# Optimization experiments

Measured on AMD Instinct MI355X. Metric: run time of the kernel, lower is better.

The kernel has to match this reference:

```python
import jax, jax.numpy as jnp
import numpy as np
import math

B, C, L_SEQ, PRED = 32, 21, 512, 96
D, H, DFF, NLAYERS = 512, 8, 2048, 3
E = D // H
PATCH_LEN, STRIDE, PAD = 16, 8, 8
PATCH_NUM = (L_SEQ - PATCH_LEN) // STRIDE + 2  # 64
MA = 25          # moving-average kernel of series_decomp
FACTOR = 1
TOP_K = int(FACTOR * math.log(PATCH_NUM))  # top-k delays in AutoCorrelation


def _pos_embedding(max_len, d_model):
    pos = np.arange(max_len, dtype=np.float32)[:, None]
    div = np.exp(np.arange(0, d_model, 2, dtype=np.float32) * -(math.log(10000.0) / d_model))
    pe = np.zeros((max_len, d_model), np.float32)
    pe[:, 0::2] = np.sin(pos * div)
    pe[:, 1::2] = np.cos(pos * div)
    return jnp.asarray(pe)

POS_EMB = _pos_embedding(PATCH_NUM, D)


def setup_inputs():
    key = jax.random.key(0)
    ks = iter(jax.random.split(key, 48))
    g = lambda shape, s=0.02: jax.random.normal(next(ks), shape, jnp.float32) * s
    inp = {"x_enc": jax.random.normal(next(ks), (B, L_SEQ, C), jnp.float32)}
    inp["w_val"] = g((PATCH_LEN, D))  # PatchEmbedding value_embedding (no bias)
    for tag in ("ac", "sa"):
        for nm in ("Wq", "Wk", "Wv", "Wo"):
            inp[nm + "_" + tag] = g((NLAYERS, D, D))
        for nm in ("bq", "bk", "bv", "bo"):
            inp[nm + "_" + tag] = g((NLAYERS, D))
    inp["Wf"] = g((NLAYERS, 2 * D, D))
    inp["bf"] = g((NLAYERS, D))
    inp["W1"] = g((NLAYERS, D, DFF))   # conv1 (1x1, no bias)
    inp["W2"] = g((NLAYERS, DFF, D))   # conv2 (1x1, no bias)
    inp["bn_g"] = jnp.ones((D,), jnp.float32)
    inp["bn_b"] = jnp.zeros((D,), jnp.float32)
    inp["W_head"] = g((D * PATCH_NUM, PRED))
    inp["b_head"] = g((PRED,))
    return inp


def _proj_heads(x, W, b):
    N, L, _ = x.shape
    return (x @ W + b).reshape(N, L, H, E)


def _auto_corr(x, Wq, bq, Wk, bk, Wv, bv, Wo, bo):
    # AutoCorrelation (training-mode time_delay_agg): FFT correlation + top-k roll aggregation
    N, L, _ = x.shape
    q = _proj_heads(x, Wq, bq)
    k = _proj_heads(x, Wk, bk)
    v = _proj_heads(x, Wv, bv)
    qf = jnp.fft.rfft(q.transpose(0, 2, 3, 1), axis=-1)   # [N,H,E,Lf]
    kf = jnp.fft.rfft(k.transpose(0, 2, 3, 1), axis=-1)
    corr = jnp.fft.irfft(qf * jnp.conj(kf), n=L, axis=-1)  # [N,H,E,L]
    vals = v.transpose(0, 2, 3, 1)                          # [N,H,E,L]
    mean_corr = corr.mean(axis=(1, 2))                      # [N,L]
    _, top_idx = jax.lax.top_k(mean_corr.mean(axis=0), TOP_K)  # delays shared across batch
    w = jax.nn.softmax(mean_corr[:, top_idx], axis=-1)      # [N,TOP_K]
    rolled = jax.vmap(lambda s: jnp.roll(vals, -s, axis=-1))(top_idx)  # [K,N,H,E,L]
    agg = jnp.einsum('knhel,nk->nhel', rolled, w)
    return agg.transpose(0, 3, 1, 2).reshape(N, L, D) @ Wo + bo


def _full_attn(x, Wq, bq, Wk, bk, Wv, bv, Wo, bo):
    N, L, _ = x.shape
    q = _proj_heads(x, Wq, bq)
    k = _proj_heads(x, Wk, bk)
    v = _proj_heads(x, Wv, bv)
    scores = jnp.einsum('blhe,bshe->bhls', q, k) / math.sqrt(E)
    out = jnp.einsum('bhls,bshe->blhe', jax.nn.softmax(scores, axis=-1), v)
    return out.reshape(N, L, D) @ Wo + bo


def _decomp(x):
    # series_decomp: residual after edge-replicated moving average (returns seasonal part)
    half = (MA - 1) // 2
    xp = jnp.concatenate([jnp.repeat(x[:, :1], half, axis=1), x,
                          jnp.repeat(x[:, -1:], half, axis=1)], axis=1)
    cs = jnp.cumsum(xp, axis=1)
    cs = jnp.concatenate([jnp.zeros_like(cs[:, :1]), cs], axis=1)
    mean = (cs[:, MA:] - cs[:, :-MA]) / MA
    return x - mean


def _forward(x_enc, w_val, Wq_ac, bq_ac, Wk_ac, bk_ac, Wv_ac, bv_ac, Wo_ac, bo_ac,
             Wq_sa, bq_sa, Wk_sa, bk_sa, Wv_sa, bv_sa, Wo_sa, bo_sa,
             Wf, bf, W1, W2, bn_g, bn_b, W_head, b_head):
    # instance normalization over time
    means = x_enc.mean(axis=1, keepdims=True)                 # [B,1,C]
    xc = x_enc - means
    stdev = jnp.sqrt(xc.var(axis=1, keepdims=True) + 1e-5)    # [B,1,C]
    xn = xc / stdev
    # patch embedding (channel independent): replication-pad end, unfold, linear + pos emb
    xp = xn.transpose(0, 2, 1)                                # [B,C,L]
    xp = jnp.concatenate([xp, jnp.repeat(xp[..., -1:], PAD, axis=-1)], axis=-1)
    idx = jnp.arange(PATCH_NUM)[:, None] * STRIDE + jnp.arange(PATCH_LEN)[None, :]
    patches = xp[..., idx]                                    # [B,C,P,patch_len]
    x = patches.reshape(B * C, PATCH_NUM, PATCH_LEN) @ w_val + POS_EMB  # [B*C,P,D]
    # hybrid encoder layers
    for l in range(NLAYERS):
        a = _auto_corr(x, Wq_ac[l], bq_ac[l], Wk_ac[l], bk_ac[l], Wv_ac[l], bv_ac[l], Wo_ac[l], bo_ac[l])
        s = _full_attn(x, Wq_sa[l], bq_sa[l], Wk_sa[l], bk_sa[l], Wv_sa[l], bv_sa[l], Wo_sa[l], bo_sa[l])
        fused = jnp.concatenate([a, s], axis=-1) @ Wf[l] + bf[l]
        x = _decomp(x + fused)
        y = jax.nn.relu(x @ W1[l]) @ W2[l]                    # 1x1 convs == pointwise linears
        x = _decomp(x + y)
    # final BatchNorm1d over d_model channels (batch statistics, affine)
    mu = x.mean(axis=(0, 1))
    var = x.var(axis=(0, 1))
    x = (x - mu) / jnp.sqrt(var + 1e-5) * bn_g + bn_b
    # head: [B*C,P,D] -> [B,C,D,P] -> flat (d-major) -> pred_len
    enc = x.reshape(B, C, PATCH_NUM, D).transpose(0, 1, 3, 2).reshape(B, C, D * PATCH_NUM)
    dec = (enc @ W_head + b_head).transpose(0, 2, 1)          # [B,PRED,C]
    return dec * stdev[:, 0][:, None, :] + means[:, 0][:, None, :]


def reference(x_enc, w_val, Wq_ac, bq_ac, Wk_ac, bk_ac, Wv_ac, bv_ac, Wo_ac, bo_ac,
              Wq_sa, bq_sa, Wk_sa, bk_sa, Wv_sa, bv_sa, Wo_sa, bo_sa,
              Wf, bf, W1, W2, bn_g, bn_b, W_head, b_head):
    return _forward(x_enc, w_val, Wq_ac, bq_ac, Wk_ac, bk_ac, Wv_ac, bv_ac, Wo_ac, bo_ac,
                    Wq_sa, bq_sa, Wk_sa, bk_sa, Wv_sa, bv_sa, Wo_sa, bo_sa,
                    Wf, bf, W1, W2, bn_g, bn_b, W_head, b_head)
```

## Files before the change

kernel.cpp:

```cpp
#include <hip/hip_runtime.h>
#include <math.h>


typedef unsigned short u16;
typedef short s16x8 __attribute__((ext_vector_type(8)));
typedef u16 u16x8 __attribute__((ext_vector_type(8)));
typedef float f32x4 __attribute__((ext_vector_type(4)));

#define MROWS 43008
#define NSEQ  672

__device__ __forceinline__ float bf2f(u16 b) {
  union { unsigned u; float f; } v; v.u = ((unsigned)b) << 16; return v.f;
}
__device__ __forceinline__ u16 f2bf(float f) {
  union { float f; unsigned u; } v; v.f = f;
  unsigned r = v.u + 0x7FFFu + ((v.u >> 16) & 1u);
  return (u16)(r >> 16);
}

__device__ __forceinline__ void gload16(const u16* g, u16* l) {
  __builtin_amdgcn_global_load_lds(
      (const __attribute__((address_space(1))) unsigned int*)g,
      (__attribute__((address_space(3))) unsigned int*)l, 16, 0, 0);
}

__global__ __launch_bounds__(256) void zero_out_kernel(float* __restrict__ o, int n) {
  int i = blockIdx.x * 256 + threadIdx.x;
  if (i < n) o[i] = 0.f;
}

__global__ __launch_bounds__(256) void transpose_cvt_b(
    const float* __restrict__ W, u16* __restrict__ Wt, int K, int N,
    long long sW, long long sT) {
  __shared__ float t[32][33];
  int z = blockIdx.z;
  W += (size_t)z * sW;
  Wt += (size_t)z * sT;
  int k0 = blockIdx.x * 32, n0 = blockIdx.y * 32;
  int tx = threadIdx.x, ty = threadIdx.y;
#pragma unroll
  for (int i = 0; i < 32; i += 8)
    t[ty + i][tx] = W[(size_t)(k0 + ty + i) * N + n0 + tx];
  __syncthreads();
#pragma unroll
  for (int i = 0; i < 32; i += 8)
    Wt[(size_t)(n0 + ty + i) * K + k0 + tx] = f2bf(t[tx][ty + i]);
}

__global__ __launch_bounds__(256) void transpose_cvt_six(
    const float* __restrict__ Wq_sa, const float* __restrict__ Wk_sa,
    const float* __restrict__ Wv_sa, const float* __restrict__ Wq_ac,
    const float* __restrict__ Wk_ac, const float* __restrict__ Wv_ac,
    u16* __restrict__ dst) {
  __shared__ float t[32][33];
  int z = blockIdx.z;
  int l = z / 6, wi = z % 6;
  const float* srcs[6] = {Wq_sa, Wk_sa, Wv_sa, Wq_ac, Wk_ac, Wv_ac};
  const float* W = srcs[wi] + (size_t)l * 262144;
  u16* out = dst + ((size_t)l * 6 + wi) * 262144;
  int k0 = blockIdx.x * 32, n0 = blockIdx.y * 32;
  int tx = threadIdx.x, ty = threadIdx.y;
#pragma unroll
  for (int i = 0; i < 32; i += 8)
    t[ty + i][tx] = W[(size_t)(k0 + ty + i) * 512 + n0 + tx];
  __syncthreads();
#pragma unroll
  for (int i = 0; i < 32; i += 8)
    out[(size_t)(n0 + ty + i) * 512 + k0 + tx] = f2bf(t[tx][ty + i]);
}

__global__ __launch_bounds__(256) void cvt_bf16_nine(
    const float* __restrict__ Wo_ac, const float* __restrict__ Wo_sa,
    const float* __restrict__ Wv_ac, u16* __restrict__ dst) {
  int z = blockIdx.z;
  int l = z / 3, s = z % 3;
  const float* base = (s == 0) ? Wo_ac : (s == 1 ? Wo_sa : Wv_ac);
  const float* src = base + (size_t)l * 262144;
  u16* out = dst + ((size_t)l * 3 + s) * 262144;
  int i = blockIdx.x * 256 + threadIdx.x;
  if (i < 262144) out[i] = f2bf(src[i]);
}

__global__ __launch_bounds__(512) void boa_eff_kernel(
    const float* __restrict__ Wo_ac, const float* __restrict__ bo_ac,
    const float* __restrict__ bv_ac, float* __restrict__ out) {
  int l = blockIdx.x;
  int i = threadIdx.x;
  const float* Wo = Wo_ac + (size_t)l * 262144;
  float s = bo_ac[l * 512 + i];
  for (int k = 0; k < 512; k++) s += bv_ac[l * 512 + k] * Wo[(size_t)k * 512 + i];
  out[l * 512 + i] = s;
}

__global__ __launch_bounds__(512) void bias_combine(
    const float* __restrict__ WfW, const float* __restrict__ bfW,
    const float* __restrict__ boa_eff, const float* __restrict__ bo_sa,
    float* __restrict__ out) {
  int l = blockIdx.x;
  const float* Wf = WfW + (size_t)l * 524288;
  int n = threadIdx.x;
  float s = bfW[l * 512 + n];
  for (int i = 0; i < 512; i++) s += boa_eff[l * 512 + i] * Wf[(size_t)i * 512 + n];
  for (int i = 0; i < 512; i++) s += bo_sa[l * 512 + i] * Wf[(size_t)(512 + i) * 512 + n];
  out[l * 512 + n] = s;
}

__global__ __launch_bounds__(512) void gemm256p(
    const u16* __restrict__ A1, const u16* __restrict__ A2, int lda, int ksplit,
    const u16* __restrict__ Bt, int ldb,
    const float* __restrict__ b0, const float* __restrict__ b1,
    const float* __restrict__ b2,
    u16* __restrict__ C, int ldc, int K, int relu, int nb) {
  __shared__ u16 smA[2][2][256 * 32];
  __shared__ u16 smB[2][2][256 * 32];
  int g = blockIdx.x;
  if ((gridDim.x & 7) == 0) g = (g & 7) * (gridDim.x >> 3) + (g >> 3);
  int m0 = (g / nb) * 256, n0 = (g % nb) * 256;
  int tid = threadIdx.x, lane = tid & 63, wid = tid >> 6;
  int wr = wid >> 2, wc = wid & 3;
  int m_in = lane & 15, kq = lane >> 4;
  int srow0 = lane >> 2, sslot = lane & 3;

  f32x4 acc[8][4];
#pragma unroll
  for (int i = 0; i < 8; i++)
#pragma unroll
    for (int j = 0; j < 4; j++) acc[i][j] = (f32x4){0.f, 0.f, 0.f, 0.f};

  int nt = K >> 6;

  auto STAGE = [&](int tp, int t, int kh) {
    int k0 = t * 64 + kh * 32;
    const u16* Ap; int kk;
    if (t * 64 < ksplit) { Ap = A1; kk = k0; } else { Ap = A2; kk = k0 - ksplit; }
#pragma unroll
    for (int i = 0; i < 2; i++) {
      int r = i * 128 + wid * 16 + srow0;
      int gs = (sslot ^ ((r >> 1) & 3)) * 8;
      gload16(&Ap[(size_t)(m0 + r) * lda + kk + gs],
              &smA[tp][kh][(i * 128 + wid * 16) * 32]);
      gload16(&Bt[(size_t)(n0 + r) * ldb + k0 + gs],
              &smB[tp][kh][(i * 128 + wid * 16) * 32]);
    }
  };

  STAGE(0, 0, 0);
  STAGE(0, 0, 1);
  asm volatile("s_waitcnt vmcnt(4)" ::: "memory");
  asm volatile("s_barrier" ::: "memory");

  int tp = 0;
  for (int t = 0; t < nt; ++t) {
    int tn = t + 1 < nt ? t + 1 : t;
#pragma unroll
    for (int kh = 0; kh < 2; kh++) {
      const u16* As = &smA[tp][kh][0];
      const u16* Bs = &smB[tp][kh][0];
      s16x8 a_[8], b_[4];
#pragma unroll
      for (int mf = 0; mf < 8; mf++) {
        int row = wr * 128 + mf * 16 + m_in;
        a_[mf] = *(const s16x8*)&As[row * 32 + ((kq ^ ((row >> 1) & 3)) * 8)];
      }
#pragma unroll
      for (int nf = 0; nf < 4; nf++) {
        int row = wc * 64 + nf * 16 + m_in;
        b_[nf] = *(const s16x8*)&Bs[row * 32 + ((kq ^ ((row >> 1) & 3)) * 8)];
      }
      STAGE(tp ^ 1, tn, kh);
      asm volatile("s_waitcnt vmcnt(4)" ::: "memory");
      asm volatile("s_barrier" ::: "memory");
      __builtin_amdgcn_s_setprio(1);
#pragma unroll
      for (int mf = 0; mf < 8; mf++)
#pragma unroll
        for (int nf = 0; nf < 4; nf++)
          acc[mf][nf] = __builtin_amdgcn_mfma_f32_16x16x32_bf16(
              a_[mf], b_[nf], acc[mf][nf], 0, 0, 0);
      __builtin_amdgcn_s_setprio(0);
    }
    tp ^= 1;
  }
  int r0 = m0 + wr * 128 + (kq << 2);
#pragma unroll
  for (int mf = 0; mf < 8; mf++) {
#pragma unroll
    for (int nf = 0; nf < 4; nf++) {
      int col = n0 + wc * 64 + nf * 16 + m_in;
      const float* bp = (col < 512) ? b0 : (col < 1024 ? b1 : b2);
      float bv = bp ? bp[col & 511] : 0.f;
#pragma unroll
      for (int r = 0; r < 4; r++) {
        float v = acc[mf][nf][r] + bv;
        if (relu) v = fmaxf(v, 0.f);
        C[(size_t)(r0 + mf * 16 + r) * ldc + col] = f2bf(v);
      }
    }
  }
}

__global__ __launch_bounds__(256) void gemm128p(
    const u16* __restrict__ A1, const u16* __restrict__ A2, int lda, int ksplit,
    const u16* __restrict__ Bt, int ldb,
    const float* __restrict__ b0, const float* __restrict__ b1,
    const float* __restrict__ b2,
    u16* __restrict__ C, int ldc, int K, int relu, int nb) {
  __shared__ u16 sm[3][8192];
  int g = blockIdx.x;
  if ((gridDim.x & 7) == 0) g = (g & 7) * (gridDim.x >> 3) + (g >> 3);
  int m0 = (g / nb) * 128, n0 = (g % nb) * 128;
  int tid = threadIdx.x, lane = tid & 63, w = tid >> 6;
  int wr = w >> 1, wc = w & 1;
  int srow = w * 16 + (lane >> 2);
  int scol = (((lane & 3) ^ ((lane >> 3) & 3)) * 8);
  int m_in = lane & 15;
  int sgrp = lane >> 4;
  int offA[4], offB[4];
#pragma unroll
  for (int mf = 0; mf < 4; mf++) {
    int row = wr * 64 + mf * 16 + m_in;
    offA[mf] = row * 32 + ((sgrp ^ ((row >> 1) & 3)) * 8);
  }
#pragma unroll
  for (int nf = 0; nf < 4; nf++) {
    int row = wc * 64 + nf * 16 + m_in;
    offB[nf] = 4096 + row * 32 + ((sgrp ^ ((row >> 1) & 3)) * 8);
  }
  f32x4 acc[4][4];
#pragma unroll
  for (int i = 0; i < 4; i++)
#pragma unroll
    for (int j = 0; j < 4; j++) acc[i][j] = (f32x4){0.f, 0.f, 0.f, 0.f};

  int nt = K >> 5;
  auto STAGE = [&](int b, int t) {
    int k0 = t * 32;
    const u16* Ab; int kk;
    if (k0 < ksplit) { Ab = A1; kk = k0; } else { Ab = A2; kk = k0 - ksplit; }
    u16* base = &sm[b][0];
    gload16(&Ab[(size_t)(m0 + srow) * lda + kk + scol],      base + w * 512);
    gload16(&Ab[(size_t)(m0 + 64 + srow) * lda + kk + scol], base + 2048 + w * 512);
    gload16(&Bt[(size_t)(n0 + srow) * ldb + k0 + scol],      base + 4096 + w * 512);
    gload16(&Bt[(size_t)(n0 + 64 + srow) * ldb + k0 + scol], base + 6144 + w * 512);
  };

  STAGE(0, 0);
  STAGE(1, 1 < nt ? 1 : nt - 1);
  int cb = 0;
  for (int t = 0; t < nt; ++t) {
    int pf = t + 2 < nt ? t + 2 : nt - 1;
    int pb = cb + 2 >= 3 ? cb - 1 : cb + 2;
    STAGE(pb, pf);
    asm volatile("s_waitcnt vmcnt(8)" ::: "memory");
    asm volatile("s_barrier" ::: "memory");
    const u16* lb = &sm[cb][0];
    s16x8 a_[4], b_[4];
#pragma unroll
    for (int mf = 0; mf < 4; mf++) a_[mf] = *(const s16x8*)&lb[offA[mf]];
#pragma unroll
    for (int nf = 0; nf < 4; nf++) b_[nf] = *(const s16x8*)&lb[offB[nf]];
    __builtin_amdgcn_s_setprio(1);
#pragma unroll
    for (int mf = 0; mf < 4; mf++)
#pragma unroll
      for (int nf = 0; nf < 4; nf++)
        acc[mf][nf] = __builtin_amdgcn_mfma_f32_16x16x32_bf16(
            a_[mf], b_[nf], acc[mf][nf], 0, 0, 0);
    __builtin_amdgcn_s_setprio(0);
    asm volatile("s_barrier" ::: "memory");
    cb = cb + 1 >= 3 ? 0 : cb + 1;
  }
  int r0 = m0 + wr * 64 + (sgrp << 2);
  int cl = lane & 15;
#pragma unroll
  for (int mf = 0; mf < 4; mf++) {
#pragma unroll
    for (int nf = 0; nf < 4; nf++) {
      int col = n0 + wc * 64 + nf * 16 + cl;
      const float* bp = (col < 512) ? b0 : (col < 1024 ? b1 : b2);
      float bv = bp ? bp[col & 511] : 0.f;
#pragma unroll
      for (int r = 0; r < 4; r++) {
        float v = acc[mf][nf][r] + bv;
        if (relu) v = fmaxf(v, 0.f);
        C[(size_t)(r0 + mf * 16 + r) * ldc + col] = f2bf(v);
      }
    }
  }
}

__global__ __launch_bounds__(256) void gram_mc_kernel(
    const u16* __restrict__ Q, const u16* __restrict__ K, int ld,
    float* __restrict__ MC) {
  __shared__ u16 lA[64][40];
  __shared__ u16 lB[64][40];
  __shared__ float red[64];
  int n = blockIdx.x;
  int tid = threadIdx.x, lane = tid & 63, w = tid >> 6;
  int sr = tid >> 2, scol = (tid & 3) * 8;
  if (tid < 64) red[tid] = 0.f;
  f32x4 acc[4];
#pragma unroll
  for (int i = 0; i < 4; i++) acc[i] = (f32x4){0.f, 0.f, 0.f, 0.f};
  size_t base = (size_t)n * 64 * ld;
  for (int k0 = 0; k0 < 512; k0 += 32) {
    *(u16x8*)&lA[sr][scol] = *(const u16x8*)&Q[base + (size_t)sr * ld + k0 + scol];
    *(u16x8*)&lB[sr][scol] = *(const u16x8*)&K[base + (size_t)sr * ld + k0 + scol];
    __syncthreads();
    int ar = w * 16 + (lane & 15);
    int kk = (lane >> 4) * 8;
    s16x8 af = *(const s16x8*)&lA[ar][kk];
#pragma unroll
    for (int nb = 0; nb < 4; nb++) {
      s16x8 bfr = *(const s16x8*)&lB[nb * 16 + (lane & 15)][kk];
      acc[nb] = __builtin_amdgcn_mfma_f32_16x16x32_bf16(af, bfr, acc[nb], 0, 0, 0);
    }
    __syncthreads();
  }
  int row0 = w * 16 + ((lane >> 4) << 2);
  int cl = lane & 15;
#pragma unroll
  for (int nb = 0; nb < 4; nb++) {
    int col = nb * 16 + cl;
#pragma unroll
    for (int r = 0; r < 4; r++)
      atomicAdd(&red[(row0 + r - col) & 63], acc[nb][r]);
  }
  __syncthreads();
  if (tid < 64) MC[n * 64 + tid] = red[tid] * (1.f / 512.f);
}

__global__ __launch_bounds__(256) void instnorm_kernel(
    const float* __restrict__ xe, float* __restrict__ MEANS, float* __restrict__ STDEV) {
  int n = blockIdx.x;
  int b = n / 21, c = n % 21;
  int tid = threadIdx.x;
  float v0 = xe[((size_t)b * 512 + tid) * 21 + c];
  float v1 = xe[((size_t)b * 512 + tid + 256) * 21 + c];
  float s = v0 + v1, ss = v0 * v0 + v1 * v1;
  for (int o = 32; o; o >>= 1) { s += __shfl_down(s, o); ss += __shfl_down(ss, o); }
  __shared__ float rs[4], rss[4];
  if ((tid & 63) == 0) { rs[tid >> 6] = s; rss[tid >> 6] = ss; }
  __syncthreads();
  if (tid == 0) {
    s = rs[0] + rs[1] + rs[2] + rs[3];
    ss = rss[0] + rss[1] + rss[2] + rss[3];
    float mean = s * (1.f / 512.f);
    float var = ss * (1.f / 512.f) - mean * mean;
    MEANS[n] = mean;
    STDEV[n] = sqrtf(var + 1e-5f);
  }
}

__global__ __launch_bounds__(256) void pe_kernel(float* __restrict__ PE) {
  int i = blockIdx.x * 256 + threadIdx.x;
  int p = i >> 9, d = i & 511;
  int k = d >> 1;
  float freq = expf(-(float)(2 * k) * (9.210340371976184f / 512.f));
  float ang = (float)p * freq;
  PE[i] = (d & 1) ? cosf(ang) : sinf(ang);
}

__global__ __launch_bounds__(256) void patch_kernel(
    const float* __restrict__ xe, const float* __restrict__ wv,
    const float* __restrict__ PE, const float* __restrict__ MEANS,
    const float* __restrict__ STDEV, u16* __restrict__ X) {
  __shared__ float pw[16][512];
  __shared__ float pat[8][16];
  int bx = blockIdx.x;
  int n = bx >> 3, pb = bx & 7;
  int b = n / 21, c = n % 21;
  int tid = threadIdx.x;
  float mean = MEANS[n], inv = 1.f / STDEV[n];
  for (int i = tid; i < 8192; i += 256) pw[i >> 9][i & 511] = wv[i];
  if (tid < 128) {
    int pp = tid >> 4, j = tid & 15;
    int l = (pb * 8 + pp) * 8 + j;
    if (l > 511) l = 511;
    pat[pp][j] = (xe[((size_t)b * 512 + l) * 21 + c] - mean) * inv;
  }
  __syncthreads();
  for (int i = tid; i < 4096; i += 256) {
    int pp = i >> 9, d = i & 511;
    int p = pb * 8 + pp;
    float s = PE[p * 512 + d];
#pragma unroll
    for (int j = 0; j < 16; j++) s += pat[pp][j] * pw[j][d];
    X[((size_t)n * 64 + p) * 512 + d] = f2bf(s);
  }
}

__global__ __launch_bounds__(256) void topk_softw_kernel(
    const float* __restrict__ MC, int* __restrict__ TIDX, float* __restrict__ WSM) {
  __shared__ float g[256];
  __shared__ float gt[64];
  __shared__ int dly[4];
  int tid = threadIdx.x;
  int tau = tid & 63, part = tid >> 6;
  float s = 0.f;
  for (int n = part * 168; n < (part + 1) * 168; n++) s += MC[n * 64 + tau];
  g[tid] = s;
  __syncthreads();
  if (tid < 64) gt[tid] = g[tid] + g[64 + tid] + g[128 + tid] + g[192 + tid];
  __syncthreads();
  if (tid == 0) {
    for (int j = 0; j < 4; j++) {
      int best = 0; float bv = -1e30f;
      for (int t = 0; t < 64; t++) if (gt[t] > bv) { bv = gt[t]; best = t; }
      dly[j] = best;
      TIDX[j] = best;
      gt[best] = -1e30f;
    }
  }
  __syncthreads();
  for (int n = tid; n < 672; n += 256) {
    float v[4], mx = -1e30f;
#pragma unroll
    for (int j = 0; j < 4; j++) { v[j] = MC[n * 64 + dly[j]]; mx = fmaxf(mx, v[j]); }
    float ssum = 0.f;
#pragma unroll
    for (int j = 0; j < 4; j++) { v[j] = __expf(v[j] - mx); ssum += v[j]; }
    float inv = 1.f / ssum;
#pragma unroll
    for (int j = 0; j < 4; j++) WSM[n * 4 + j] = v[j] * inv;
  }
}

__global__ __launch_bounds__(256) void agg_kernel(
    const u16* __restrict__ V, int ldv, const float* __restrict__ WSM,
    const int* __restrict__ TIDX, u16* __restrict__ OUT, int ldo) {
  int n = blockIdx.x;
  __shared__ float w[4];
  __shared__ int dly[4];
  int tid = threadIdx.x;
  if (tid < 4) { w[tid] = WSM[n * 4 + tid]; dly[tid] = TIDX[tid]; }
  __syncthreads();
  for (int i = tid; i < 64 * 512; i += 256) {
    int l = i >> 9, d = i & 511;
    float s = 0.f;
#pragma unroll
    for (int j = 0; j < 4; j++)
      s += w[j] * bf2f(V[((size_t)n * 64 + ((l + dly[j]) & 63)) * ldv + d]);
    OUT[((size_t)n * 64 + l) * ldo + d] = f2bf(s);
  }
}

__global__ __launch_bounds__(256) void attn_mfma(u16* __restrict__ QKV) {
  __shared__ u16 lq[64][72], lk[64][72], lvt[64][72], lp[64][72];
  int n = blockIdx.x >> 3, h = blockIdx.x & 7;
  size_t base = (size_t)n * 64 * 1536;
  int qo = h * 64, ko = 512 + h * 64, vo = 1024 + h * 64;
  int tid = threadIdx.x, lane = tid & 63, w = tid >> 6;
  int r = tid >> 2, c0 = (tid & 3) * 16;
  *(u16x8*)&lq[r][c0]     = *(const u16x8*)&QKV[base + (size_t)r * 1536 + qo + c0];
  *(u16x8*)&lq[r][c0 + 8] = *(const u16x8*)&QKV[base + (size_t)r * 1536 + qo + c0 + 8];
  *(u16x8*)&lk[r][c0]     = *(const u16x8*)&QKV[base + (size_t)r * 1536 + ko + c0];
  *(u16x8*)&lk[r][c0 + 8] = *(const u16x8*)&QKV[base + (size_t)r * 1536 + ko + c0 + 8];
  u16x8 v0 = *(const u16x8*)&QKV[base + (size_t)r * 1536 + vo + c0];
  u16x8 v1 = *(const u16x8*)&QKV[base + (size_t)r * 1536 + vo + c0 + 8];
#pragma unroll
  for (int j = 0; j < 8; j++) { lvt[c0 + j][r] = v0[j]; lvt[c0 + 8 + j][r] = v1[j]; }
  __syncthreads();
  int m_in = lane & 15, ks = (lane >> 4) * 8;
  int rq = lane >> 4;
  s16x8 aq0 = *(const s16x8*)&lq[w * 16 + m_in][ks];
  s16x8 aq1 = *(const s16x8*)&lq[w * 16 + m_in][32 + ks];
  f32x4 s4[4];
#pragma unroll
  for (int nf = 0; nf < 4; nf++) {
    s4[nf] = (f32x4){0.f, 0.f, 0.f, 0.f};
    s16x8 b0 = *(const s16x8*)&lk[nf * 16 + m_in][ks];
    s16x8 b1 = *(const s16x8*)&lk[nf * 16 + m_in][32 + ks];
    s4[nf] = __builtin_amdgcn_mfma_f32_16x16x32_bf16(aq0, b0, s4[nf], 0, 0, 0);
    s4[nf] = __builtin_amdgcn_mfma_f32_16x16x32_bf16(aq1, b1, s4[nf], 0, 0, 0);
  }
  float mx[4] = {-1e30f, -1e30f, -1e30f, -1e30f};
#pragma unroll
  for (int nf = 0; nf < 4; nf++)
#pragma unroll
    for (int r4 = 0; r4 < 4; r4++) {
      s4[nf][r4] *= 0.125f;
      mx[r4] = fmaxf(mx[r4], s4[nf][r4]);
    }
#pragma unroll
  for (int o = 1; o < 16; o <<= 1)
#pragma unroll
    for (int r4 = 0; r4 < 4; r4++) mx[r4] = fmaxf(mx[r4], __shfl_xor(mx[r4], o));
  float sum[4] = {0.f, 0.f, 0.f, 0.f};
#pragma unroll
  for (int nf = 0; nf < 4; nf++)
#pragma unroll
    for (int r4 = 0; r4 < 4; r4++) {
      float e = __expf(s4[nf][r4] - mx[r4]);
      s4[nf][r4] = e;
      sum[r4] += e;
    }
#pragma unroll
  for (int o = 1; o < 16; o <<= 1)
#pragma unroll
    for (int r4 = 0; r4 < 4; r4++) sum[r4] += __shfl_xor(sum[r4], o);
#pragma unroll
  for (int nf = 0; nf < 4; nf++)
#pragma unroll
    for (int r4 = 0; r4 < 4; r4++)
      lp[w * 16 + rq * 4 + r4][nf * 16 + m_in] = f2bf(s4[nf][r4] / sum[r4]);
  __syncthreads();
  s16x8 ap0 = *(const s16x8*)&lp[w * 16 + m_in][ks];
  s16x8 ap1 = *(const s16x8*)&lp[w * 16 + m_in][32 + ks];
#pragma unroll
  for (int nf = 0; nf < 4; nf++) {
    f32x4 o4 = (f32x4){0.f, 0.f, 0.f, 0.f};
    s16x8 b0 = *(const s16x8*)&lvt[nf * 16 + m_in][ks];
    s16x8 b1 = *(const s16x8*)&lvt[nf * 16 + m_in][32 + ks];
    o4 = __builtin_amdgcn_mfma_f32_16x16x32_bf16(ap0, b0, o4, 0, 0, 0);
    o4 = __builtin_amdgcn_mfma_f32_16x16x32_bf16(ap1, b1, o4, 0, 0, 0);
#pragma unroll
    for (int r4 = 0; r4 < 4; r4++)
      QKV[base + (size_t)(w * 16 + rq * 4 + r4) * 1536 + qo + nf * 16 + m_in] =
          f2bf(o4[r4]);
  }
}

__global__ __launch_bounds__(256) void decomp_kernel(
    u16* __restrict__ X, const u16* __restrict__ DELTA, int ds) {
  int n = blockIdx.x >> 1;
  int d = ((blockIdx.x & 1) << 8) + threadIdx.x;
  size_t xb = ((size_t)n * 64) * 512 + d;
  size_t db = ((size_t)n * 64) * ds + d;
  float v[64];
#pragma unroll
  for (int l = 0; l < 64; l++)
    v[l] = bf2f(X[xb + (size_t)l * 512]) + bf2f(DELTA[db + (size_t)l * ds]);
  float s = 12.f * v[0];
#pragma unroll
  for (int t = 0; t <= 12; t++) s += v[t];
#pragma unroll
  for (int l = 0; l < 64; l++) {
    float out = v[l] - s * (1.f / 25.f);
    X[xb + (size_t)l * 512] = f2bf(out);
    if (l < 63) {
      int add = l + 13; if (add > 63) add = 63;
      int sub = l - 12; if (sub < 0) sub = 0;
      s += v[add] - v[sub];
    }
  }
}

__global__ __launch_bounds__(256) void bn_part(
    const u16* __restrict__ X, float* __restrict__ PS) {
  int ch = blockIdx.x, tid = threadIdx.x;
  float s1a = 0, s2a = 0, s1b = 0, s2b = 0;
  size_t base = (size_t)ch * 128 * 512;
  for (int r = 0; r < 128; r++) {
    float a = bf2f(X[base + (size_t)r * 512 + tid]);
    float b = bf2f(X[base + (size_t)r * 512 + tid + 256]);
    s1a += a; s2a += a * a; s1b += b; s2b += b * b;
  }
  PS[(size_t)(ch * 2 + 0) * 512 + tid] = s1a;
  PS[(size_t)(ch * 2 + 0) * 512 + tid + 256] = s1b;
  PS[(size_t)(ch * 2 + 1) * 512 + tid] = s2a;
  PS[(size_t)(ch * 2 + 1) * 512 + tid + 256] = s2b;
}

__global__ __launch_bounds__(256) void bn_final(
    const float* __restrict__ PS, const float* __restrict__ g,
    const float* __restrict__ b, float* __restrict__ SCALE, float* __restrict__ SHIFT) {
  int d = blockIdx.x * 256 + threadIdx.x;
  float s = 0, ss = 0;
  for (int c = 0; c < 336; c++) {
    s += PS[(size_t)(c * 2) * 512 + d];
    ss += PS[(size_t)(c * 2 + 1) * 512 + d];
  }
  float mu = s * (1.f / 43008.f);
  float var = ss * (1.f / 43008.f) - mu * mu;
  float inv = 1.f / sqrtf(var + 1e-5f);
  float sc = g[d] * inv;
  SCALE[d] = sc;
  SHIFT[d] = b[d] - mu * sc;
}

__global__ __launch_bounds__(256) void bn_transpose_kernel(
    const u16* __restrict__ X, const float* __restrict__ SCALE,
    const float* __restrict__ SHIFT, u16* __restrict__ ENC) {
  __shared__ u16 t[64][72];
  int n = blockIdx.x >> 3, dc = (blockIdx.x & 7) * 64;
  int tid = threadIdx.x;
  for (int i = tid; i < 4096; i += 256) {
    int p = i >> 6, d = i & 63;
    float v = bf2f(X[((size_t)n * 64 + p) * 512 + dc + d]) * SCALE[dc + d] + SHIFT[dc + d];
    t[p][d] = f2bf(v);
  }
  __syncthreads();
  for (int i = tid; i < 4096; i += 256) {
    int d = i >> 6, p = i & 63;
    ENC[(size_t)n * 32768 + (size_t)(dc + d) * 64 + p] = t[p][d];
  }
}

__global__ __launch_bounds__(256) void head_gemm(
    const u16* __restrict__ ENC, const u16* __restrict__ Wht,
    float* __restrict__ PART) {
  __shared__ u16 lA[64][40];
  __shared__ u16 lB[96][40];
  int bm = blockIdx.x;
  int kc = blockIdx.y;
  int tid = threadIdx.x, lane = tid & 63, w = tid >> 6;
  int sr = tid >> 2, sc0 = (tid & 3) * 8;
  f32x4 acc[6];
#pragma unroll
  for (int i = 0; i < 6; i++) acc[i] = (f32x4){0.f, 0.f, 0.f, 0.f};
  for (int kk0 = 0; kk0 < 2048; kk0 += 32) {
    int k0 = kc * 2048 + kk0;
    *(u16x8*)&lA[sr][sc0] =
        *(const u16x8*)&ENC[(size_t)(bm * 64 + sr) * 32768 + k0 + sc0];
    for (int i = tid; i < 96 * 4; i += 256) {
      int rB = i >> 2, seg = (i & 3) * 8;
      *(u16x8*)&lB[rB][seg] = *(const u16x8*)&Wht[(size_t)rB * 32768 + k0 + seg];
    }
    __syncthreads();
    int ar = w * 16 + (lane & 15);
    int kk = (lane >> 4) * 8;
    s16x8 af = *(const s16x8*)&lA[ar][kk];
#pragma unroll
    for (int nb = 0; nb < 6; nb++) {
      s16x8 bfr = *(const s16x8*)&lB[nb * 16 + (lane & 15)][kk];
      acc[nb] = __builtin_amdgcn_mfma_f32_16x16x32_bf16(af, bfr, acc[nb], 0, 0, 0);
    }
    __syncthreads();
  }
  int rb = bm * 64 + w * 16 + ((lane >> 4) << 2);
  int cl = lane & 15;
#pragma unroll
  for (int nb = 0; nb < 6; nb++) {
    int col = nb * 16 + cl;
#pragma unroll
    for (int r = 0; r < 4; r++) {
      int row = rb + r;
      if (row < 672) PART[((size_t)kc * 672 + row) * 96 + col] = acc[nb][r];
    }
  }
}

__global__ __launch_bounds__(256) void head_reduce(
    const float* __restrict__ PART, const float* __restrict__ bh,
    const float* __restrict__ STDEV, const float* __restrict__ MEANS,
    float* __restrict__ OUT) {
  int i = blockIdx.x * 256 + threadIdx.x;
  if (i >= 672 * 96) return;
  int n = i / 96, r = i % 96;
  float s = bh[r];
  for (int kc = 0; kc < 16; kc++) s += PART[((size_t)kc * 672 + n) * 96 + r];
  int b = n / 21, c = n % 21;
  OUT[((size_t)b * 96 + r) * 21 + c] = s * STDEV[n] + MEANS[n];
}

extern "C" void kernel_launch(void* const* d_in, const int* in_sizes, int n_in,
                              void* d_out, int out_size, void* d_ws, size_t ws_size,
                              hipStream_t stream) {
  const float* x_enc = (const float*)d_in[0];
  const float* w_val = (const float*)d_in[1];
  const float* Wq_ac = (const float*)d_in[2];
  const float* Wk_ac = (const float*)d_in[3];
  const float* Wv_ac = (const float*)d_in[4];
  const float* Wo_ac = (const float*)d_in[5];
  const float* bq_ac = (const float*)d_in[6];
  const float* bk_ac = (const float*)d_in[7];
  const float* bv_ac = (const float*)d_in[8];
  const float* bo_ac = (const float*)d_in[9];
  const float* Wq_sa = (const float*)d_in[10];
  const float* Wk_sa = (const float*)d_in[11];
  const float* Wv_sa = (const float*)d_in[12];
  const float* Wo_sa = (const float*)d_in[13];
  const float* bq_sa = (const float*)d_in[14];
  const float* bk_sa = (const float*)d_in[15];
  const float* bv_sa = (const float*)d_in[16];
  const float* bo_sa = (const float*)d_in[17];
  const float* WfW   = (const float*)d_in[18];
  const float* bfW   = (const float*)d_in[19];
  const float* W1    = (const float*)d_in[20];
  const float* W2    = (const float*)d_in[21];
  const float* bn_g  = (const float*)d_in[22];
  const float* bn_b  = (const float*)d_in[23];
  const float* W_head = (const float*)d_in[24];
  const float* b_head = (const float*)d_in[25];
  (void)in_sizes; (void)n_in; (void)out_size;

  char* wsp = (char*)d_ws;
  size_t off = 0;
  auto alloc = [&](size_t bytes) -> void* {
    void* p = wsp + off;
    off += (bytes + 255) & ~(size_t)255;
    return p;
  };
  u16* X    = (u16*)alloc((size_t)MROWS * 512 * 2);
  u16* Q3   = (u16*)alloc((size_t)MROWS * 1536 * 2);
  u16* SIX   = (u16*)alloc((size_t)3 * 6 * 262144 * 2);
  u16* W1T   = (u16*)alloc((size_t)3 * 1048576 * 2);
  u16* W2T   = (u16*)alloc((size_t)3 * 1048576 * 2);
  u16* WFT   = (u16*)alloc((size_t)3 * 524288 * 2);
  u16* WORIG = (u16*)alloc((size_t)3 * 3 * 262144 * 2);
  u16* WCOMB = (u16*)alloc((size_t)3 * 524288 * 2);
  u16* WHT   = (u16*)alloc((size_t)3145728 * 2);
  u16* TMP   = (u16*)alloc((size_t)262144 * 2);
  float* PE = (float*)alloc((size_t)32768 * 4);
  float* MEANS = (float*)alloc(672 * 4);
  float* STDEV = (float*)alloc(672 * 4);
  float* MC = (float*)alloc(672 * 64 * 4);
  int* TIDX = (int*)alloc(4 * 4);
  float* WSM = (float*)alloc(672 * 4 * 4);
  float* BNP = (float*)alloc((size_t)336 * 1024 * 4);
  float* SCALE = (float*)alloc(512 * 4);
  float* SHIFT = (float*)alloc(512 * 4);
  float* BOAE = (float*)alloc(3 * 512 * 4);
  float* BCOMB = (float*)alloc(3 * 512 * 4);
  u16* C0 = Q3;
  u16* C1 = Q3 + 512;
  u16* C2 = Q3 + 1024;
  u16* HBUF = Q3;
  u16* YBUF = Q3 + (size_t)21504 * 2048;
  u16* ENC  = Q3;
  float* HEADP = (float*)X;

  if (off > ws_size) {
    zero_out_kernel<<<252, 256, 0, stream>>>((float*)d_out, 672 * 96);
    return;
  }

  transpose_cvt_six<<<dim3(16, 16, 18), dim3(32, 8), 0, stream>>>(
      Wq_sa, Wk_sa, Wv_sa, Wq_ac, Wk_ac, Wv_ac, SIX);
  transpose_cvt_b<<<dim3(16, 64, 3), dim3(32, 8), 0, stream>>>(
      W1, W1T, 512, 2048, 1048576, 1048576);
  transpose_cvt_b<<<dim3(64, 16, 3), dim3(32, 8), 0, stream>>>(
      W2, W2T, 2048, 512, 1048576, 1048576);
  transpose_cvt_b<<<dim3(32, 16, 3), dim3(32, 8), 0, stream>>>(
      WfW, WFT, 1024, 512, 524288, 524288);
  transpose_cvt_b<<<dim3(1024, 3, 1), dim3(32, 8), 0, stream>>>(
      W_head, WHT, 32768, 96, 0, 0);
  cvt_bf16_nine<<<dim3(1024, 1, 9), 256, 0, stream>>>(Wo_ac, Wo_sa, Wv_ac, WORIG);
  boa_eff_kernel<<<3, 512, 0, stream>>>(Wo_ac, bo_ac, bv_ac, BOAE);
  bias_combine<<<3, 512, 0, stream>>>(WfW, bfW, BOAE, bo_sa, BCOMB);
  for (int l = 0; l < 3; l++) {
    const u16* wfT = WFT + (size_t)l * 524288;
    const u16* woa = WORIG + (size_t)l * 3 * 262144;
    const u16* wos = woa + 262144;
    const u16* wva = woa + 2 * 262144;
    u16* wc = WCOMB + (size_t)l * 524288;
    gemm128p<<<16, 256, 0, stream>>>(
        wfT, wfT, 1024, 512, woa, 512,
        nullptr, nullptr, nullptr, TMP, 512, 512, 0, 4);
    gemm128p<<<16, 256, 0, stream>>>(
        TMP, TMP, 512, 512, wva, 512,
        nullptr, nullptr, nullptr, wc, 1024, 512, 0, 4);
    gemm128p<<<16, 256, 0, stream>>>(
        wfT + 512, wfT + 512, 1024, 512, wos, 512,
        nullptr, nullptr, nullptr, wc + 512, 1024, 512, 0, 4);
  }

  instnorm_kernel<<<672, 256, 0, stream>>>(x_enc, MEANS, STDEV);
  pe_kernel<<<128, 256, 0, stream>>>(PE);
  patch_kernel<<<672 * 8, 256, 0, stream>>>(x_enc, w_val, PE, MEANS, STDEV, X);

  auto g256 = [&](const u16* A1, const u16* A2, int lda, int ksplit,
                  const u16* Bt, int ldb, const float* b0, const float* b1,
                  const float* b2, u16* C, int ldc, int M, int N, int K,
                  int relu) {
    int nb = N / 256;
    gemm256p<<<(M / 256) * nb, 512, 0, stream>>>(
        A1, A2, lda, ksplit, Bt, ldb, b0, b1, b2, C, ldc, K, relu, nb);
  };

  for (int l = 0; l < 3; l++) {
    const u16* qkv_sa = SIX + (size_t)l * 6 * 262144;
    const u16* qk_ac  = qkv_sa + (size_t)3 * 262144;
    const u16* w1     = W1T + (size_t)l * 1048576;
    const u16* w2     = W2T + (size_t)l * 1048576;
    const u16* wcomb  = WCOMB + (size_t)l * 524288;
    g256(X, X, 512, 512, qkv_sa, 512, bq_sa + l * 512, bk_sa + l * 512,
         bv_sa + l * 512, Q3, 1536, MROWS, 1536, 512, 0);
    attn_mfma<<<5376, 256, 0, stream>>>(Q3);
    g256(X, X, 512, 512, qk_ac, 512, bq_ac + l * 512, bk_ac + l * 512, nullptr,
         C1, 1536, MROWS, 1024, 512, 0);
    gram_mc_kernel<<<672, 256, 0, stream>>>(C1, C2, 1536, MC);
    topk_softw_kernel<<<1, 256, 0, stream>>>(MC, TIDX, WSM);
    agg_kernel<<<672, 256, 0, stream>>>(X, 512, WSM, TIDX, C2, 1536);
    g256(C2, C0, 1536, 512, wcomb, 1024, BCOMB + l * 512, nullptr, nullptr,
         C1, 1536, MROWS, 512, 1024, 0);
    decomp_kernel<<<1344, 256, 0, stream>>>(X, C1, 1536);
    for (int c = 0; c < 2; c++) {
      const u16* Xc = X + (size_t)c * 21504 * 512;
      u16* Yc = YBUF + (size_t)c * 21504 * 512;
      g256(Xc, Xc, 512, 512, w1, 512, nullptr, nullptr, nullptr,
           HBUF, 2048, 21504, 2048, 512, 1);
      gemm128p<<<672, 256, 0, stream>>>(
          HBUF, HBUF, 2048, 2048, w2, 2048, nullptr, nullptr, nullptr,
          Yc, 512, 2048, 0, 4);
    }
    decomp_kernel<<<1344, 256, 0, stream>>>(X, YBUF, 512);
  }

  bn_part<<<336, 256, 0, stream>>>(X, BNP);
  bn_final<<<2, 256, 0, stream>>>(BNP, bn_g, bn_b, SCALE, SHIFT);
  bn_transpose_kernel<<<672 * 8, 256, 0, stream>>>(X, SCALE, SHIFT, ENC);
  head_gemm<<<dim3(11, 16), 256, 0, stream>>>(ENC, WHT, HEADP);
  head_reduce<<<252, 256, 0, stream>>>(HEADP, b_head, STDEV, MEANS, (float*)d_out);
}
```

Baseline: 2.279 ms.

## Replace 256x256 GEMM with 128x256 tile and triple-buffered K=32 pipeline

The big GEMM kernel moves from a 256x256 tile with double-buffered K=64 stages to a 128x256 tile with a three-stage ring of K=32 LDS buffers. Prefetch now runs two stages ahead and LDS fragment offsets are precomputed. The smaller tile and reduced accumulator and LDS footprint (launch_bounds 512,4) aim for more resident blocks and better latency hiding. The cost is lower arithmetic intensity per tile, more global traffic for the B matrix, and an extra barrier per K step.

New measurement: 2.290 ms. Within noise of the previous version (+0.5%).

```diff
diff --git a/kernel.cpp b/kernel.cpp
--- a/kernel.cpp
+++ b/kernel.cpp
@@ -106,85 +106,81 @@
   out[l * 512 + n] = s;
 }
 
-__global__ __launch_bounds__(512) void gemm256p(
+__global__ __launch_bounds__(512, 4) void gemm128x256(
     const u16* __restrict__ A1, const u16* __restrict__ A2, int lda, int ksplit,
     const u16* __restrict__ Bt, int ldb,
     const float* __restrict__ b0, const float* __restrict__ b1,
     const float* __restrict__ b2,
     u16* __restrict__ C, int ldc, int K, int relu, int nb) {
-  __shared__ u16 smA[2][2][256 * 32];
-  __shared__ u16 smB[2][2][256 * 32];
+  __shared__ u16 smA[3][128 * 32];
+  __shared__ u16 smB[3][256 * 32];
   int g = blockIdx.x;
   if ((gridDim.x & 7) == 0) g = (g & 7) * (gridDim.x >> 3) + (g >> 3);
-  int m0 = (g / nb) * 256, n0 = (g % nb) * 256;
+  int m0 = (g / nb) * 128, n0 = (g % nb) * 256;
   int tid = threadIdx.x, lane = tid & 63, wid = tid >> 6;
   int wr = wid >> 2, wc = wid & 3;
   int m_in = lane & 15, kq = lane >> 4;
-  int srow0 = lane >> 2, sslot = lane & 3;
-
-  f32x4 acc[8][4];
-#pragma unroll
-  for (int i = 0; i < 8; i++)
+  int sr = tid >> 2;
+  int gsl = (((tid & 3) ^ ((sr >> 1) & 3)) * 8);
+
+  int offA[4], offB[4];
+#pragma unroll
+  for (int mf = 0; mf < 4; mf++) {
+    int row = wr * 64 + mf * 16 + m_in;
+    offA[mf] = row * 32 + ((kq ^ ((row >> 1) & 3)) * 8);
+  }
+#pragma unroll
+  for (int nf = 0; nf < 4; nf++) {
+    int row = wc * 64 + nf * 16 + m_in;
+    offB[nf] = row * 32 + ((kq ^ ((row >> 1) & 3)) * 8);
+  }
+  f32x4 acc[4][4];
+#pragma unroll
+  for (int i = 0; i < 4; i++)
 #pragma unroll
     for (int j = 0; j < 4; j++) acc[i][j] = (f32x4){0.f, 0.f, 0.f, 0.f};
 
-  int nt = K >> 6;
-
-  auto STAGE = [&](int tp, int t, int kh) {
-    int k0 = t * 64 + kh * 32;
+  int nt = K >> 5;
+  auto STAGE = [&](int b, int t) {
+    int k0 = t * 32;
     const u16* Ap; int kk;
-    if (t * 64 < ksplit) { Ap = A1; kk = k0; } else { Ap = A2; kk = k0 - ksplit; }
-#pragma unroll
-    for (int i = 0; i < 2; i++) {
-      int r = i * 128 + wid * 16 + srow0;
-      int gs = (sslot ^ ((r >> 1) & 3)) * 8;
-      gload16(&Ap[(size_t)(m0 + r) * lda + kk + gs],
-              &smA[tp][kh][(i * 128 + wid * 16) * 32]);
-      gload16(&Bt[(size_t)(n0 + r) * ldb + k0 + gs],
-              &smB[tp][kh][(i * 128 + wid * 16) * 32]);
-    }
+    if (k0 < ksplit) { Ap = A1; kk = k0; } else { Ap = A2; kk = k0 - ksplit; }
+    gload16(&Ap[(size_t)(m0 + sr) * lda + kk + gsl], &smA[b][wid * 512]);
+    gload16(&Bt[(size_t)(n0 + sr) * ldb + k0 + gsl], &smB[b][wid * 512]);
+    gload16(&Bt[(size_t)(n0 + 128 + sr) * ldb + k0 + gsl],
+            &smB[b][4096 + wid * 512]);
   };
 
-  STAGE(0, 0, 0);
-  STAGE(0, 0, 1);
-  asm volatile("s_waitcnt vmcnt(4)" ::: "memory");
-  asm volatile("s_barrier" ::: "memory");
-
-  int tp = 0;
+  STAGE(0, 0);
+  STAGE(1, 1 < nt ? 1 : nt - 1);
+  int cb = 0;
   for (int t = 0; t < nt; ++t) {
-    int tn = t + 1 < nt ? t + 1 : t;
-#pragma unroll
-    for (int kh = 0; kh < 2; kh++) {
-      const u16* As = &smA[tp][kh][0];
-      const u16* Bs = &smB[tp][kh][0];
-      s16x8 a_[8], b_[4];
-#pragma unroll
-      for (int mf = 0; mf < 8; mf++) {
-        int row = wr * 128 + mf * 16 + m_in;
-        a_[mf] = *(const s16x8*)&As[row * 32 + ((kq ^ ((row >> 1) & 3)) * 8)];
-      }
-#pragma unroll
-      for (int nf = 0; nf < 4; nf++) {
-        int row = wc * 64 + nf * 16 + m_in;
-        b_[nf] = *(const s16x8*)&Bs[row * 32 + ((kq ^ ((row >> 1) & 3)) * 8)];
-      }
-      STAGE(tp ^ 1, tn, kh);
-      asm volatile("s_waitcnt vmcnt(4)" ::: "memory");
-      asm volatile("s_barrier" ::: "memory");
-      __builtin_amdgcn_s_setprio(1);
-#pragma unroll
-      for (int mf = 0; mf < 8; mf++)
-#pragma unroll
-        for (int nf = 0; nf < 4; nf++)
-          acc[mf][nf] = __builtin_amdgcn_mfma_f32_16x16x32_bf16(
-              a_[mf], b_[nf], acc[mf][nf], 0, 0, 0);
-      __builtin_amdgcn_s_setprio(0);
-    }
-    tp ^= 1;
-  }
-  int r0 = m0 + wr * 128 + (kq << 2);
-#pragma unroll
-  for (int mf = 0; mf < 8; mf++) {
+    int pf = t + 2 < nt ? t + 2 : nt - 1;
+    int pb = cb + 2 >= 3 ? cb - 1 : cb + 2;
+    STAGE(pb, pf);
+    asm volatile("s_waitcnt vmcnt(6)" ::: "memory");
+    asm volatile("s_barrier" ::: "memory");
+    const u16* la = &smA[cb][0];
+    const u16* lb = &smB[cb][0];
+    s16x8 a_[4], b_[4];
+#pragma unroll
+    for (int mf = 0; mf < 4; mf++) a_[mf] = *(const s16x8*)&la[offA[mf]];
+#pragma unroll
+    for (int nf = 0; nf < 4; nf++) b_[nf] = *(const s16x8*)&lb[offB[nf]];
+    __builtin_amdgcn_s_setprio(1);
+#pragma unroll
+    for (int mf = 0; mf < 4; mf++)
+#pragma unroll
+      for (int nf = 0; nf < 4; nf++)
+        acc[mf][nf] = __builtin_amdgcn_mfma_f32_16x16x32_bf16(
+            a_[mf], b_[nf], acc[mf][nf], 0, 0, 0);
+    __builtin_amdgcn_s_setprio(0);
+    asm volatile("s_barrier" ::: "memory");
+    cb = cb + 1 >= 3 ? 0 : cb + 1;
+  }
+  int r0 = m0 + wr * 64 + (kq << 2);
+#pragma unroll
+  for (int mf = 0; mf < 4; mf++) {
 #pragma unroll
     for (int nf = 0; nf < 4; nf++) {
       int col = n0 + wc * 64 + nf * 16 + m_in;
@@ -761,12 +757,12 @@
   pe_kernel<<<128, 256, 0, stream>>>(PE);
   patch_kernel<<<672 * 8, 256, 0, stream>>>(x_enc, w_val, PE, MEANS, STDEV, X);
 
-  auto g256 = [&](const u16* A1, const u16* A2, int lda, int ksplit,
+  auto gbig = [&](const u16* A1, const u16* A2, int lda, int ksplit,
                   const u16* Bt, int ldb, const float* b0, const float* b1,
                   const float* b2, u16* C, int ldc, int M, int N, int K,
                   int relu) {
     int nb = N / 256;
-    gemm256p<<<(M / 256) * nb, 512, 0, stream>>>(
+    gemm128x256<<<(M / 128) * nb, 512, 0, stream>>>(
         A1, A2, lda, ksplit, Bt, ldb, b0, b1, b2, C, ldc, K, relu, nb);
   };
 
@@ -776,21 +772,21 @@
     const u16* w1     = W1T + (size_t)l * 1048576;
     const u16* w2     = W2T + (size_t)l * 1048576;
     const u16* wcomb  = WCOMB + (size_t)l * 524288;
-    g256(X, X, 512, 512, qkv_sa, 512, bq_sa + l * 512, bk_sa + l * 512,
+    gbig(X, X, 512, 512, qkv_sa, 512, bq_sa + l * 512, bk_sa + l * 512,
          bv_sa + l * 512, Q3, 1536, MROWS, 1536, 512, 0);
     attn_mfma<<<5376, 256, 0, stream>>>(Q3);
-    g256(X, X, 512, 512, qk_ac, 512, bq_ac + l * 512, bk_ac + l * 512, nullptr,
+    gbig(X, X, 512, 512, qk_ac, 512, bq_ac + l * 512, bk_ac + l * 512, nullptr,
          C1, 1536, MROWS, 1024, 512, 0);
     gram_mc_kernel<<<672, 256, 0, stream>>>(C1, C2, 1536, MC);
     topk_softw_kernel<<<1, 256, 0, stream>>>(MC, TIDX, WSM);
     agg_kernel<<<672, 256, 0, stream>>>(X, 512, WSM, TIDX, C2, 1536);
-    g256(C2, C0, 1536, 512, wcomb, 1024, BCOMB + l * 512, nullptr, nullptr,
+    gbig(C2, C0, 1536, 512, wcomb, 1024, BCOMB + l * 512, nullptr, nullptr,
          C1, 1536, MROWS, 512, 1024, 0);
     decomp_kernel<<<1344, 256, 0, stream>>>(X, C1, 1536);
     for (int c = 0; c < 2; c++) {
       const u16* Xc = X + (size_t)c * 21504 * 512;
       u16* Yc = YBUF + (size_t)c * 21504 * 512;
-      g256(Xc, Xc, 512, 512, w1, 512, nullptr, nullptr, nullptr,
+      gbig(Xc, Xc, 512, 512, w1, 512, nullptr, nullptr, nullptr,
            HBUF, 2048, 21504, 2048, 512, 1);
       gemm128p<<<672, 256, 0, stream>>>(
           HBUF, HBUF, 2048, 2048, w2, 2048, nullptr, nullptr, nullptr,
```
